# Kernel tuning notes

Measured on AMD Instinct MI355X. Metric: run time of the kernel, lower is better.

Reference implementation:

```python
import jax, jax.numpy as jnp
import numpy as np

KH, KW = 3, 3
PAD = 1
STRIDE = 1


def dht1(x):
    # 1D Discrete Hartley Transform along last axis: Re(FFT) - Im(FFT)
    f = jnp.fft.fft(x, axis=-1)
    return f.real - f.imag


def dht2(x, fft_h, fft_w):
    # zero-pad trailing two dims up to (fft_h, fft_w), then DHT along w then h
    pad_h = fft_h - x.shape[-2]
    pad_w = fft_w - x.shape[-1]
    pads = [(0, 0)] * (x.ndim - 2) + [(0, pad_h), (0, pad_w)]
    x = jnp.pad(x, pads)
    x = dht1(x)
    x = jnp.swapaxes(dht1(jnp.swapaxes(x, -1, -2)), -1, -2)
    return x


def setup_inputs() -> dict:
    key = jax.random.key(0)
    k1, k2 = jax.random.split(key)
    x = jax.random.normal(k1, (8, 64, 128, 128), dtype=jnp.float32)
    weight = jax.random.normal(k2, (64, 64, KH, KW), dtype=jnp.float32)
    return {"x": x, "weight": weight}


def reference(x, weight):
    b, c_in, h, w = x.shape
    out_h = (h + 2 * PAD - KH) // STRIDE + 1
    out_w = (w + 2 * PAD - KW) // STRIDE + 1
    x_p = jnp.pad(x, ((0, 0), (0, 0), (PAD, PAD), (PAD, PAD)))
    fft_h = h + 2 * PAD + KH - 1
    fft_w = w + 2 * PAD + KW - 1

    x_ht = dht2(x_p, fft_h, fft_w)          # [B, Cin, fh, fw]
    w_ht = dht2(weight, fft_h, fft_w)        # [Cout, Cin, fh, fw]

    x_f = jnp.flip(x_ht, axis=(-2, -1))
    w_f = jnp.flip(w_ht, axis=(-2, -1))

    # Fused combine + sum over Cin: avoids [B,Cout,Cin,fh,fw] intermediates.
    t1 = jnp.einsum('bchw,ochw->bohw', x_ht, w_ht)
    t2 = jnp.einsum('bchw,ochw->bohw', x_ht, w_f)
    t3 = jnp.einsum('bchw,ochw->bohw', x_f, w_ht)
    t4 = jnp.einsum('bchw,ochw->bohw', x_f, w_f)
    out_ht = (t1 + t2 + t3 - t4) * 0.5

    # idht2 in the source applies only the 1/n scaling twice (no transform)
    output = out_ht / jnp.asarray(fft_h * fft_w, dtype=out_ht.dtype)
    return output[:, :, :out_h, :out_w]
```

## Files before the change

### kernel.cpp

```cpp
#include <hip/hip_runtime.h>
#include <hip/hip_fp16.h>


#define SCALE (0.5f / 17424.0f)
#define MFMA  __builtin_amdgcn_mfma_f32_16x16x32_f16

typedef __attribute__((ext_vector_type(8))) _Float16 f16x8;
typedef __attribute__((ext_vector_type(4))) _Float16 f16x4;
typedef __attribute__((ext_vector_type(4))) float    f32x4;

static __device__ __forceinline__ f16x8 scl(f16x8 a, _Float16 s) {
    #pragma unroll
    for (int e = 0; e < 8; ++e) a[e] *= s;
    return a;
}

__global__ __launch_bounds__(256) void build_all(
    const float* __restrict__ w, _Float16* __restrict__ Tf,
    _Float16* __restrict__ cfT, _Float16* __restrict__ hgT)
{
    const int bid = blockIdx.x;
    const int tid = threadIdx.x;
    const float step = 6.28318530717958647692f / 132.0f;
    if (bid < 144) {
        if (tid < 128) {
            float val = 0.f;
            if (bid < 132) {
                const int m = (bid * (tid + 1)) % 132;
                float s, c;
                sincosf((float)m * step, &s, &c);
                val = c + s;
            }
            Tf[bid * 128 + tid] = (_Float16)val;
        }
        return;
    }
    if (bid == 144) {
        if (tid < 128) {
            const int v = tid;
            float s, c;
            _Float16 o[8];
            o[0] = (_Float16)1.0f; o[3] = (_Float16)1.0f;
            o[6] = (_Float16)0.0f; o[7] = (_Float16)0.0f;
            sincosf((float)((v * 1) % 132) * step, &s, &c);       o[1] = (_Float16)(c + s);
            sincosf((float)((v * 2) % 132) * step, &s, &c);       o[2] = (_Float16)(c + s);
            sincosf((float)(((v + 1) * 1) % 132) * step, &s, &c); o[4] = (_Float16)(c - s);
            sincosf((float)(((v + 1) * 2) % 132) * step, &s, &c); o[5] = (_Float16)(c - s);
            *(f16x8*)(cfT + v * 8) = *(f16x8*)o;
        }
        return;
    }
    const int bid2 = bid - 145;
    const int u = bid2 >> 2;
    const int itbase = (bid2 & 3) * 4;
    float a[3], ap[3];
    a[0] = 1.f; ap[0] = 1.f;
    #pragma unroll
    for (int i = 1; i < 3; ++i) {
        float s, c;
        sincosf((float)((u * i) % 132) * step, &s, &c);
        a[i] = c + s;
        sincosf((float)(((u + 1) * i) % 132) * step, &s, &c);
        ap[i] = c - s;
    }
    for (int it = itbase; it < itbase + 4; ++it) {
        const int oc = it * 256 + tid;
        const float* wp = w + (size_t)oc * 9;
        float w9[9];
        #pragma unroll
        for (int q = 0; q < 9; ++q) w9[q] = wp[q];
        #pragma unroll
        for (int j = 0; j < 3; ++j) {
            const float h = a[0]*w9[j] + a[1]*w9[3+j] + a[2]*w9[6+j];
            const float g = ap[0]*w9[j] + ap[1]*w9[3+j] + ap[2]*w9[6+j];
            hgT[((size_t)u * 6 + j)     * 4096 + oc] = (_Float16)h;
            hgT[((size_t)u * 6 + 3 + j) * 4096 + oc] = (_Float16)g;
        }
    }
}

__global__ __launch_bounds__(256, 2) void dht2_fused(
    const float* __restrict__ x, const _Float16* __restrict__ Tf,
    _Float16* __restrict__ X)
{
    const int bc = blockIdx.x;
    const int tid = threadIdx.x, wv = tid >> 6, lane = tid & 63;
    const int col = lane & 15, quad = lane >> 4;
    __shared__ _Float16 Tfl[144][136];
    __shared__ _Float16 Y1l[144][136];

    const float* xp = x + (size_t)bc * 16384;

    float4 xv[2][4][2];
    #pragma unroll
    for (int nt = 0; nt < 2; ++nt) {
        const int ic = (wv * 2 + nt) * 16 + col;
        #pragma unroll
        for (int kc = 0; kc < 4; ++kc) {
            const int k0 = kc * 32 + quad * 8;
            xv[nt][kc][0] = *(const float4*)(xp + ic * 128 + k0);
            xv[nt][kc][1] = *(const float4*)(xp + ic * 128 + k0 + 4);
        }
    }
    #pragma unroll
    for (int s = 0; s < 9; ++s) {
        const int idx = tid + 256 * s;
        const int row = idx >> 4;
        const int ce  = (idx & 15) * 8;
        *(f16x8*)&Tfl[row][ce] = *(const f16x8*)(Tf + (size_t)idx * 8);
    }
    f16x8 bfA[2][4];
    #pragma unroll
    for (int nt = 0; nt < 2; ++nt)
        #pragma unroll
        for (int kc = 0; kc < 4; ++kc) {
            f16x8 t;
            t[0] = (_Float16)xv[nt][kc][0].x; t[1] = (_Float16)xv[nt][kc][0].y;
            t[2] = (_Float16)xv[nt][kc][0].z; t[3] = (_Float16)xv[nt][kc][0].w;
            t[4] = (_Float16)xv[nt][kc][1].x; t[5] = (_Float16)xv[nt][kc][1].y;
            t[6] = (_Float16)xv[nt][kc][1].z; t[7] = (_Float16)xv[nt][kc][1].w;
            bfA[nt][kc] = t;
        }
    __syncthreads();

    f32x4 accA[2][9];
    #pragma unroll
    for (int nt = 0; nt < 2; ++nt)
        #pragma unroll
        for (int mt = 0; mt < 9; ++mt) accA[nt][mt] = (f32x4)0.f;
    #pragma unroll
    for (int kc = 0; kc < 4; ++kc) {
        const int k0 = kc * 32 + quad * 8;
        #pragma unroll
        for (int mt = 0; mt < 9; ++mt) {
            const f16x8 af = *(const f16x8*)&Tfl[mt * 16 + col][k0];
            accA[0][mt] = MFMA(af, bfA[0][kc], accA[0][mt], 0, 0, 0);
            accA[1][mt] = MFMA(af, bfA[1][kc], accA[1][mt], 0, 0, 0);
        }
    }
    #pragma unroll
    for (int nt = 0; nt < 2; ++nt) {
        const int ic = (wv * 2 + nt) * 16 + col;
        #pragma unroll
        for (int mt = 0; mt < 9; ++mt)
            #pragma unroll
            for (int r = 0; r < 4; ++r)
                Y1l[mt * 16 + quad * 4 + r][ic] = (_Float16)accA[nt][mt][r];
    }
    __syncthreads();

    f32x4 accB[3][9];
    #pragma unroll
    for (int t = 0; t < 3; ++t)
        #pragma unroll
        for (int mt = 0; mt < 9; ++mt) accB[t][mt] = (f32x4)0.f;
    #pragma unroll
    for (int kc = 0; kc < 4; ++kc) {
        const int k0 = kc * 32 + quad * 8;
        f16x8 af9[9];
        #pragma unroll
        for (int mt = 0; mt < 9; ++mt)
            af9[mt] = *(const f16x8*)&Tfl[mt * 16 + col][k0];
        #pragma unroll
        for (int t = 0; t < 3; ++t) {
            const int nt = wv + 4 * t;
            if (nt < 9) {
                const f16x8 bf = *(const f16x8*)&Y1l[nt * 16 + col][k0];
                #pragma unroll
                for (int mt = 0; mt < 9; ++mt)
                    accB[t][mt] = MFMA(af9[mt], bf, accB[t][mt], 0, 0, 0);
            }
        }
    }

    __syncthreads();
    #pragma unroll
    for (int t = 0; t < 3; ++t) {
        const int nt = wv + 4 * t;
        if (nt < 9) {
            const int vg = nt * 16 + col;
            if (vg < 132) {
                #pragma unroll
                for (int mt = 0; mt < 9; ++mt)
                    #pragma unroll
                    for (int r = 0; r < 4; ++r) {
                        const int u = mt * 16 + quad * 4 + r;
                        if (u < 132) Tfl[u][vg] = (_Float16)accB[t][mt][r];
                    }
            }
        }
    }
    __syncthreads();
    _Float16* Xp = X + (size_t)bc * 17952;
    #pragma unroll
    for (int k = 0; k < 9; ++k) {
        const int ch = tid + 256 * k;
        if (ch < 2244) {
            const int u = ch / 17, kk = ch - u * 17;
            *(f16x8*)(Xp + u * 136 + kk * 8) = *(const f16x8*)&Tfl[u][kk * 8];
        }
    }
}

__global__ __launch_bounds__(256) void combine_mfma(
    const _Float16* __restrict__ X, const _Float16* __restrict__ hgT,
    const _Float16* __restrict__ cfT, float* __restrict__ out)
{
    const int uidx = blockIdx.x;
    const int b = blockIdx.y;
    const int tid = threadIdx.x;
    const int wv = tid >> 6, lane = tid & 63;
    const int col = lane & 15, quad = lane >> 4;
    const int u2 = 131 - uidx;
    const bool doB = (uidx >= 4);

    __shared__ _Float16 Ps[132][72];
    __shared__ _Float16 Ms[132][72];

    {
        const int c = tid >> 2, sub = tid & 3;
        const _Float16* rowd = X + (size_t)(b * 64 + c) * 17952 + (size_t)uidx * 136;
        const _Float16* rowm = X + (size_t)(b * 64 + c) * 17952 + (size_t)u2 * 136;
        #pragma unroll
        for (int k = 0; k < 8; ++k) {
            const int v0 = sub * 32 + 4 * k;
            const f16x4 d = *(const f16x4*)(rowd + v0);
            const f16x4 m = *(const f16x4*)(rowm + (128 - v0));
            #pragma unroll
            for (int i = 0; i < 4; ++i) {
                Ps[v0 + i][c] = d[i] + m[3 - i];
                Ms[v0 + i][c] = d[i] - m[3 - i];
            }
        }
        if (sub == 0) {
            const f16x4 d = *(const f16x4*)(rowd + 128);
            const f16x4 m = *(const f16x4*)(rowm);
            #pragma unroll
            for (int i = 0; i < 4; ++i) {
                Ps[128 + i][c] = d[i] + m[3 - i];
                Ms[128 + i][c] = d[i] - m[3 - i];
            }
        }
    }
    f16x8 cfv[8];
    #pragma unroll
    for (int nt = 0; nt < 8; ++nt)
        cfv[nt] = *(const f16x8*)(cfT + (size_t)(nt * 16 + col) * 8);

    const _Float16* hgu = hgT + (size_t)uidx * 6 * 4096;
    const int orow = wv * 16 + col;
    f16x8 hA[3][2], gA[3][2];
    #pragma unroll
    for (int kt = 0; kt < 3; ++kt)
        #pragma unroll
        for (int hf = 0; hf < 2; ++hf) {
            hA[kt][hf] = *(const f16x8*)(hgu + ((size_t)kt * 64 + orow) * 64 + hf * 32 + quad * 8);
            gA[kt][hf] = *(const f16x8*)(hgu + ((size_t)(3 + kt) * 64 + orow) * 64 + hf * 32 + quad * 8);
        }
    __syncthreads();

    float* outA = out + (((size_t)(b * 64 + wv * 16 + quad * 4)) * 128 + uidx) * 128 + col;
    float* outB = out + (((size_t)(b * 64 + wv * 16 + quad * 4)) * 128 + u2) * 128 + col;

    #pragma unroll
    for (int nt = 0; nt < 8; ++nt) {
        const int vA = nt * 16 + col;
        const int vB = 131 - vA;
        const _Float16 csP1 = cfv[nt][1], csP2 = cfv[nt][2];
        const _Float16 csM1 = cfv[nt][4], csM2 = cfv[nt][5];
        {
            const f16x8 p0 = *(const f16x8*)&Ps[vA][quad * 8];
            const f16x8 p1 = *(const f16x8*)&Ps[vA][32 + quad * 8];
            const f16x8 m0 = *(const f16x8*)&Ms[vA][quad * 8];
            const f16x8 m1 = *(const f16x8*)&Ms[vA][32 + quad * 8];
            f32x4 aP = (f32x4)0.f, aM = (f32x4)0.f;
            aP = MFMA(hA[0][0], p0, aP, 0, 0, 0);
            aP = MFMA(hA[0][1], p1, aP, 0, 0, 0);
            aM = MFMA(gA[0][0], m0, aM, 0, 0, 0);
            aM = MFMA(gA[0][1], m1, aM, 0, 0, 0);
            aP = MFMA(hA[1][0], scl(p0, csP1), aP, 0, 0, 0);
            aP = MFMA(hA[1][1], scl(p1, csP1), aP, 0, 0, 0);
            aM = MFMA(gA[1][0], scl(m0, csM1), aM, 0, 0, 0);
            aM = MFMA(gA[1][1], scl(m1, csM1), aM, 0, 0, 0);
            aP = MFMA(hA[2][0], scl(p0, csP2), aP, 0, 0, 0);
            aP = MFMA(hA[2][1], scl(p1, csP2), aP, 0, 0, 0);
            aM = MFMA(gA[2][0], scl(m0, csM2), aM, 0, 0, 0);
            aM = MFMA(gA[2][1], scl(m1, csM2), aM, 0, 0, 0);
            #pragma unroll
            for (int r = 0; r < 4; ++r)
                outA[(size_t)r * 16384 + nt * 16] = (aP[r] + aM[r]) * SCALE;
        }
        if (doB) {
            const f16x8 p0 = *(const f16x8*)&Ps[vB][quad * 8];
            const f16x8 p1 = *(const f16x8*)&Ps[vB][32 + quad * 8];
            const f16x8 m0 = *(const f16x8*)&Ms[vB][quad * 8];
            const f16x8 m1 = *(const f16x8*)&Ms[vB][32 + quad * 8];
            f32x4 bP = (f32x4)0.f, bM = (f32x4)0.f;
            bP = MFMA(gA[0][0], p0, bP, 0, 0, 0);
            bP = MFMA(gA[0][1], p1, bP, 0, 0, 0);
            bM = MFMA(hA[0][0], m0, bM, 0, 0, 0);
            bM = MFMA(hA[0][1], m1, bM, 0, 0, 0);
            bP = MFMA(gA[1][0], scl(p0, csP1), bP, 0, 0, 0);
            bP = MFMA(gA[1][1], scl(p1, csP1), bP, 0, 0, 0);
            bM = MFMA(hA[1][0], scl(m0, csM1), bM, 0, 0, 0);
            bM = MFMA(hA[1][1], scl(m1, csM1), bM, 0, 0, 0);
            bP = MFMA(gA[2][0], scl(p0, csP2), bP, 0, 0, 0);
            bP = MFMA(gA[2][1], scl(p1, csP2), bP, 0, 0, 0);
            bM = MFMA(hA[2][0], scl(m0, csM2), bM, 0, 0, 0);
            bM = MFMA(hA[2][1], scl(m1, csM2), bM, 0, 0, 0);
            #pragma unroll
            for (int r = 0; r < 4; ++r)
                outB[(size_t)r * 16384 + nt * 16] = (bP[r] - bM[r]) * SCALE;
        }
    }
}

extern "C" void kernel_launch(void* const* d_in, const int* in_sizes, int n_in,
                              void* d_out, int out_size, void* d_ws, size_t ws_size,
                              hipStream_t stream)
{
    const float* x = (const float*)d_in[0];
    const float* w = (const float*)d_in[1];
    char* ws = (char*)d_ws;
    _Float16* Tf  = (_Float16*)(ws);
    _Float16* cfT = (_Float16*)(ws + 36864);
    _Float16* X   = (_Float16*)(ws + 65536);
    _Float16* hgT = (_Float16*)(ws + 18448384);

    build_all<<<dim3(409), dim3(256), 0, stream>>>(w, Tf, cfT, hgT);

    dht2_fused<<<dim3(512), dim3(256), 0, stream>>>(x, Tf, X);

    combine_mfma<<<dim3(66, 8), dim3(256), 0, stream>>>(
        X, hgT, cfT, (float*)d_out);
}
```

Before: 114.4 us.

## Widen DHT and combine kernels to 512 threads and move twiddle scaling post-MFMA

The DHT kernel now runs 8 waves per block, one 16-column tile per wave, with the leftover 132-column tail split across the first four waves. The combine kernel packs two batches into each 512-thread block with double shared buffers. It also applies the cos/sin twiddle factors in fp32 after separate MFMA accumulators, where before it scaled fp16 inputs ahead of each MFMA. The aim is less per-thread register pressure, more waves in flight and no fp16 vector scaling, at the cost of extra accumulators and roughly double the LDS per combine block.

Result: no change. 115.5 us (+1.0%).

```diff
diff --git a/kernel.cpp b/kernel.cpp
--- a/kernel.cpp
+++ b/kernel.cpp
@@ -8,12 +8,6 @@
 typedef __attribute__((ext_vector_type(8))) _Float16 f16x8;
 typedef __attribute__((ext_vector_type(4))) _Float16 f16x4;
 typedef __attribute__((ext_vector_type(4))) float    f32x4;
-
-static __device__ __forceinline__ f16x8 scl(f16x8 a, _Float16 s) {
-    #pragma unroll
-    for (int e = 0; e < 8; ++e) a[e] *= s;
-    return a;
-}
 
 __global__ __launch_bounds__(256) void build_all(
     const float* __restrict__ w, _Float16* __restrict__ Tf,
@@ -79,7 +73,7 @@
     }
 }
 
-__global__ __launch_bounds__(256, 2) void dht2_fused(
+__global__ __launch_bounds__(512, 4) void dht2_fused(
     const float* __restrict__ x, const _Float16* __restrict__ Tf,
     _Float16* __restrict__ X)
 {
@@ -90,111 +84,109 @@
     __shared__ _Float16 Y1l[144][136];
 
     const float* xp = x + (size_t)bc * 16384;
-
-    float4 xv[2][4][2];
-    #pragma unroll
-    for (int nt = 0; nt < 2; ++nt) {
-        const int ic = (wv * 2 + nt) * 16 + col;
+    const int ic = wv * 16 + col;
+
+    float4 xv[4][2];
+    #pragma unroll
+    for (int kc = 0; kc < 4; ++kc) {
+        const int k0 = kc * 32 + quad * 8;
+        xv[kc][0] = *(const float4*)(xp + ic * 128 + k0);
+        xv[kc][1] = *(const float4*)(xp + ic * 128 + k0 + 4);
+    }
+    #pragma unroll
+    for (int s = 0; s < 5; ++s) {
+        const int idx = tid + 512 * s;
+        if (idx < 2304) {
+            const int row = idx >> 4;
+            const int ce  = (idx & 15) * 8;
+            *(f16x8*)&Tfl[row][ce] = *(const f16x8*)(Tf + (size_t)idx * 8);
+        }
+    }
+    f16x8 bfA[4];
+    #pragma unroll
+    for (int kc = 0; kc < 4; ++kc) {
+        f16x8 t;
+        t[0] = (_Float16)xv[kc][0].x; t[1] = (_Float16)xv[kc][0].y;
+        t[2] = (_Float16)xv[kc][0].z; t[3] = (_Float16)xv[kc][0].w;
+        t[4] = (_Float16)xv[kc][1].x; t[5] = (_Float16)xv[kc][1].y;
+        t[6] = (_Float16)xv[kc][1].z; t[7] = (_Float16)xv[kc][1].w;
+        bfA[kc] = t;
+    }
+    __syncthreads();
+
+    f32x4 accA[9];
+    #pragma unroll
+    for (int mt = 0; mt < 9; ++mt) accA[mt] = (f32x4)0.f;
+    #pragma unroll
+    for (int kc = 0; kc < 4; ++kc) {
+        const int k0 = kc * 32 + quad * 8;
+        #pragma unroll
+        for (int mt = 0; mt < 9; ++mt) {
+            const f16x8 af = *(const f16x8*)&Tfl[mt * 16 + col][k0];
+            accA[mt] = MFMA(af, bfA[kc], accA[mt], 0, 0, 0);
+        }
+    }
+    #pragma unroll
+    for (int mt = 0; mt < 9; ++mt)
+        #pragma unroll
+        for (int r = 0; r < 4; ++r)
+            Y1l[mt * 16 + quad * 4 + r][ic] = (_Float16)accA[mt][r];
+    __syncthreads();
+
+    f32x4 accB[9];
+    #pragma unroll
+    for (int mt = 0; mt < 9; ++mt) accB[mt] = (f32x4)0.f;
+    #pragma unroll
+    for (int kc = 0; kc < 4; ++kc) {
+        const int k0 = kc * 32 + quad * 8;
+        const f16x8 bf = *(const f16x8*)&Y1l[wv * 16 + col][k0];
+        #pragma unroll
+        for (int mt = 0; mt < 9; ++mt) {
+            const f16x8 af = *(const f16x8*)&Tfl[mt * 16 + col][k0];
+            accB[mt] = MFMA(af, bf, accB[mt], 0, 0, 0);
+        }
+    }
+    f32x4 accT[3];
+    #pragma unroll
+    for (int j = 0; j < 3; ++j) accT[j] = (f32x4)0.f;
+    if (wv < 4) {
         #pragma unroll
         for (int kc = 0; kc < 4; ++kc) {
             const int k0 = kc * 32 + quad * 8;
-            xv[nt][kc][0] = *(const float4*)(xp + ic * 128 + k0);
-            xv[nt][kc][1] = *(const float4*)(xp + ic * 128 + k0 + 4);
-        }
-    }
-    #pragma unroll
-    for (int s = 0; s < 9; ++s) {
-        const int idx = tid + 256 * s;
-        const int row = idx >> 4;
-        const int ce  = (idx & 15) * 8;
-        *(f16x8*)&Tfl[row][ce] = *(const f16x8*)(Tf + (size_t)idx * 8);
-    }
-    f16x8 bfA[2][4];
-    #pragma unroll
-    for (int nt = 0; nt < 2; ++nt)
-        #pragma unroll
-        for (int kc = 0; kc < 4; ++kc) {
-            f16x8 t;
-            t[0] = (_Float16)xv[nt][kc][0].x; t[1] = (_Float16)xv[nt][kc][0].y;
-            t[2] = (_Float16)xv[nt][kc][0].z; t[3] = (_Float16)xv[nt][kc][0].w;
-            t[4] = (_Float16)xv[nt][kc][1].x; t[5] = (_Float16)xv[nt][kc][1].y;
-            t[6] = (_Float16)xv[nt][kc][1].z; t[7] = (_Float16)xv[nt][kc][1].w;
-            bfA[nt][kc] = t;
-        }
-    __syncthreads();
-
-    f32x4 accA[2][9];
-    #pragma unroll
-    for (int nt = 0; nt < 2; ++nt)
-        #pragma unroll
-        for (int mt = 0; mt < 9; ++mt) accA[nt][mt] = (f32x4)0.f;
-    #pragma unroll
-    for (int kc = 0; kc < 4; ++kc) {
-        const int k0 = kc * 32 + quad * 8;
-        #pragma unroll
-        for (int mt = 0; mt < 9; ++mt) {
-            const f16x8 af = *(const f16x8*)&Tfl[mt * 16 + col][k0];
-            accA[0][mt] = MFMA(af, bfA[0][kc], accA[0][mt], 0, 0, 0);
-            accA[1][mt] = MFMA(af, bfA[1][kc], accA[1][mt], 0, 0, 0);
-        }
-    }
-    #pragma unroll
-    for (int nt = 0; nt < 2; ++nt) {
-        const int ic = (wv * 2 + nt) * 16 + col;
-        #pragma unroll
-        for (int mt = 0; mt < 9; ++mt)
-            #pragma unroll
-            for (int r = 0; r < 4; ++r)
-                Y1l[mt * 16 + quad * 4 + r][ic] = (_Float16)accA[nt][mt][r];
-    }
-    __syncthreads();
-
-    f32x4 accB[3][9];
-    #pragma unroll
-    for (int t = 0; t < 3; ++t)
-        #pragma unroll
-        for (int mt = 0; mt < 9; ++mt) accB[t][mt] = (f32x4)0.f;
-    #pragma unroll
-    for (int kc = 0; kc < 4; ++kc) {
-        const int k0 = kc * 32 + quad * 8;
-        f16x8 af9[9];
-        #pragma unroll
-        for (int mt = 0; mt < 9; ++mt)
-            af9[mt] = *(const f16x8*)&Tfl[mt * 16 + col][k0];
-        #pragma unroll
-        for (int t = 0; t < 3; ++t) {
-            const int nt = wv + 4 * t;
-            if (nt < 9) {
-                const f16x8 bf = *(const f16x8*)&Y1l[nt * 16 + col][k0];
+            const f16x8 bf = *(const f16x8*)&Y1l[128 + col][k0];
+            #pragma unroll
+            for (int j = 0; j < 3; ++j) {
+                if (j < 2 || wv == 0) {
+                    const int mt = (j == 2) ? 8 : (wv * 2 + j);
+                    const f16x8 af = *(const f16x8*)&Tfl[mt * 16 + col][k0];
+                    accT[j] = MFMA(af, bf, accT[j], 0, 0, 0);
+                }
+            }
+        }
+    }
+    __syncthreads();
+
+    #pragma unroll
+    for (int mt = 0; mt < 9; ++mt)
+        #pragma unroll
+        for (int r = 0; r < 4; ++r)
+            Tfl[mt * 16 + quad * 4 + r][wv * 16 + col] = (_Float16)accB[mt][r];
+    if (wv < 4 && col < 4) {
+        #pragma unroll
+        for (int j = 0; j < 3; ++j) {
+            if (j < 2 || wv == 0) {
+                const int mt = (j == 2) ? 8 : (wv * 2 + j);
                 #pragma unroll
-                for (int mt = 0; mt < 9; ++mt)
-                    accB[t][mt] = MFMA(af9[mt], bf, accB[t][mt], 0, 0, 0);
-            }
-        }
-    }
-
-    __syncthreads();
-    #pragma unroll
-    for (int t = 0; t < 3; ++t) {
-        const int nt = wv + 4 * t;
-        if (nt < 9) {
-            const int vg = nt * 16 + col;
-            if (vg < 132) {
-                #pragma unroll
-                for (int mt = 0; mt < 9; ++mt)
-                    #pragma unroll
-                    for (int r = 0; r < 4; ++r) {
-                        const int u = mt * 16 + quad * 4 + r;
-                        if (u < 132) Tfl[u][vg] = (_Float16)accB[t][mt][r];
-                    }
+                for (int r = 0; r < 4; ++r)
+                    Tfl[mt * 16 + quad * 4 + r][128 + col] = (_Float16)accT[j][r];
             }
         }
     }
     __syncthreads();
     _Float16* Xp = X + (size_t)bc * 17952;
     #pragma unroll
-    for (int k = 0; k < 9; ++k) {
-        const int ch = tid + 256 * k;
+    for (int s = 0; s < 5; ++s) {
+        const int ch = tid + 512 * s;
         if (ch < 2244) {
             const int u = ch / 17, kk = ch - u * 17;
             *(f16x8*)(Xp + u * 136 + kk * 8) = *(const f16x8*)&Tfl[u][kk * 8];
@@ -202,23 +194,27 @@
     }
 }
 
-__global__ __launch_bounds__(256) void combine_mfma(
+__global__ __launch_bounds__(512, 2) void combine_mfma(
     const _Float16* __restrict__ X, const _Float16* __restrict__ hgT,
     const _Float16* __restrict__ cfT, float* __restrict__ out)
 {
     const int uidx = blockIdx.x;
-    const int b = blockIdx.y;
     const int tid = threadIdx.x;
-    const int wv = tid >> 6, lane = tid & 63;
+    const int wv8 = tid >> 6;
+    const int half = wv8 >> 2;
+    const int wv = wv8 & 3;
+    const int lane = tid & 63;
     const int col = lane & 15, quad = lane >> 4;
+    const int b = blockIdx.y * 2 + half;
     const int u2 = 131 - uidx;
     const bool doB = (uidx >= 4);
 
-    __shared__ _Float16 Ps[132][72];
-    __shared__ _Float16 Ms[132][72];
+    __shared__ _Float16 Ps[2][132][72];
+    __shared__ _Float16 Ms[2][132][72];
 
     {
-        const int c = tid >> 2, sub = tid & 3;
+        const int th = tid & 255;
+        const int c = th >> 2, sub = th & 3;
         const _Float16* rowd = X + (size_t)(b * 64 + c) * 17952 + (size_t)uidx * 136;
         const _Float16* rowm = X + (size_t)(b * 64 + c) * 17952 + (size_t)u2 * 136;
         #pragma unroll
@@ -228,8 +224,8 @@
             const f16x4 m = *(const f16x4*)(rowm + (128 - v0));
             #pragma unroll
             for (int i = 0; i < 4; ++i) {
-                Ps[v0 + i][c] = d[i] + m[3 - i];
-                Ms[v0 + i][c] = d[i] - m[3 - i];
+                Ps[half][v0 + i][c] = d[i] + m[3 - i];
+                Ms[half][v0 + i][c] = d[i] - m[3 - i];
             }
         }
         if (sub == 0) {
@@ -237,15 +233,11 @@
             const f16x4 m = *(const f16x4*)(rowm);
             #pragma unroll
             for (int i = 0; i < 4; ++i) {
-                Ps[128 + i][c] = d[i] + m[3 - i];
-                Ms[128 + i][c] = d[i] - m[3 - i];
-            }
-        }
-    }
-    f16x8 cfv[8];
-    #pragma unroll
-    for (int nt = 0; nt < 8; ++nt)
-        cfv[nt] = *(const f16x8*)(cfT + (size_t)(nt * 16 + col) * 8);
+                Ps[half][128 + i][c] = d[i] + m[3 - i];
+                Ms[half][128 + i][c] = d[i] - m[3 - i];
+            }
+        }
+    }
 
     const _Float16* hgu = hgT + (size_t)uidx * 6 * 4096;
     const int orow = wv * 16 + col;
@@ -266,51 +258,46 @@
     for (int nt = 0; nt < 8; ++nt) {
         const int vA = nt * 16 + col;
         const int vB = 131 - vA;
-        const _Float16 csP1 = cfv[nt][1], csP2 = cfv[nt][2];
-        const _Float16 csM1 = cfv[nt][4], csM2 = cfv[nt][5];
+        const f16x8 cf8 = *(const f16x8*)(cfT + (size_t)(nt * 16 + col) * 8);
+        const float c1 = (float)cf8[1], c2 = (float)cf8[2];
+        const float d1 = (float)cf8[4], d2 = (float)cf8[5];
         {
-            const f16x8 p0 = *(const f16x8*)&Ps[vA][quad * 8];
-            const f16x8 p1 = *(const f16x8*)&Ps[vA][32 + quad * 8];
-            const f16x8 m0 = *(const f16x8*)&Ms[vA][quad * 8];
-            const f16x8 m1 = *(const f16x8*)&Ms[vA][32 + quad * 8];
-            f32x4 aP = (f32x4)0.f, aM = (f32x4)0.f;
-            aP = MFMA(hA[0][0], p0, aP, 0, 0, 0);
-            aP = MFMA(hA[0][1], p1, aP, 0, 0, 0);
-            aM = MFMA(gA[0][0], m0, aM, 0, 0, 0);
-            aM = MFMA(gA[0][1], m1, aM, 0, 0, 0);
-            aP = MFMA(hA[1][0], scl(p0, csP1), aP, 0, 0, 0);
-            aP = MFMA(hA[1][1], scl(p1, csP1), aP, 0, 0, 0);
-            aM = MFMA(gA[1][0], scl(m0, csM1), aM, 0, 0, 0);
-            aM = MFMA(gA[1][1], scl(m1, csM1), aM, 0, 0, 0);
-            aP = MFMA(hA[2][0], scl(p0, csP2), aP, 0, 0, 0);
-            aP = MFMA(hA[2][1], scl(p1, csP2), aP, 0, 0, 0);
-            aM = MFMA(gA[2][0], scl(m0, csM2), aM, 0, 0, 0);
-            aM = MFMA(gA[2][1], scl(m1, csM2), aM, 0, 0, 0);
+            const f16x8 p0 = *(const f16x8*)&Ps[half][vA][quad * 8];
+            const f16x8 p1 = *(const f16x8*)&Ps[half][vA][32 + quad * 8];
+            const f16x8 m0 = *(const f16x8*)&Ms[half][vA][quad * 8];
+            const f16x8 m1 = *(const f16x8*)&Ms[half][vA][32 + quad * 8];
+            f32x4 aP0 = (f32x4)0.f, aP1 = (f32x4)0.f, aP2 = (f32x4)0.f;
+            f32x4 aM0 = (f32x4)0.f, aM1 = (f32x4)0.f, aM2 = (f32x4)0.f;
+            aP0 = MFMA(hA[0][0], p0, aP0, 0, 0, 0); aP0 = MFMA(hA[0][1], p1, aP0, 0, 0, 0);
+            aP1 = MFMA(hA[1][0], p0, aP1, 0, 0, 0); aP1 = MFMA(hA[1][1], p1, aP1, 0, 0, 0);
+            aP2 = MFMA(hA[2][0], p0, aP2, 0, 0, 0); aP2 = MFMA(hA[2][1], p1, aP2, 0, 0, 0);
+            aM0 = MFMA(gA[0][0], m0, aM0, 0, 0, 0); aM0 = MFMA(gA[0][1], m1, aM0, 0, 0, 0);
+            aM1 = MFMA(gA[1][0], m0, aM1, 0, 0, 0); aM1 = MFMA(gA[1][1], m1, aM1, 0, 0, 0);
+            aM2 = MFMA(gA[2][0], m0, aM2, 0, 0, 0); aM2 = MFMA(gA[2][1], m1, aM2, 0, 0, 0);
             #pragma unroll
             for (int r = 0; r < 4; ++r)
-                outA[(size_t)r * 16384 + nt * 16] = (aP[r] + aM[r]) * SCALE;
+                outA[(size_t)r * 16384 + nt * 16] =
+                    ((aP0[r] + c1 * aP1[r] + c2 * aP2[r]) +
+                     (aM0[r] + d1 * aM1[r] + d2 * aM2[r])) * SCALE;
         }
         if (doB) {
-            const f16x8 p0 = *(const f16x8*)&Ps[vB][quad * 8];
-            const f16x8 p1 = *(const f16x8*)&Ps[vB][32 + quad * 8];
-            const f16x8 m0 = *(const f16x8*)&Ms[vB][quad * 8];
-            const f16x8 m1 = *(const f16x8*)&Ms[vB][32 + quad * 8];
-            f32x4 bP = (f32x4)0.f, bM = (f32x4)0.f;
-            bP = MFMA(gA[0][0], p0, bP, 0, 0, 0);
-            bP = MFMA(gA[0][1], p1, bP, 0, 0, 0);
-            bM = MFMA(hA[0][0], m0, bM, 0, 0, 0);
-            bM = MFMA(hA[0][1], m1, bM, 0, 0, 0);
-            bP = MFMA(gA[1][0], scl(p0, csP1), bP, 0, 0, 0);
-            bP = MFMA(gA[1][1], scl(p1, csP1), bP, 0, 0, 0);
-            bM = MFMA(hA[1][0], scl(m0, csM1), bM, 0, 0, 0);
-            bM = MFMA(hA[1][1], scl(m1, csM1), bM, 0, 0, 0);
-            bP = MFMA(gA[2][0], scl(p0, csP2), bP, 0, 0, 0);
-            bP = MFMA(gA[2][1], scl(p1, csP2), bP, 0, 0, 0);
-            bM = MFMA(hA[2][0], scl(m0, csM2), bM, 0, 0, 0);
-            bM = MFMA(hA[2][1], scl(m1, csM2), bM, 0, 0, 0);
+            const f16x8 p0 = *(const f16x8*)&Ps[half][vB][quad * 8];
+            const f16x8 p1 = *(const f16x8*)&Ps[half][vB][32 + quad * 8];
+            const f16x8 m0 = *(const f16x8*)&Ms[half][vB][quad * 8];
+            const f16x8 m1 = *(const f16x8*)&Ms[half][vB][32 + quad * 8];
+            f32x4 bP0 = (f32x4)0.f, bP1 = (f32x4)0.f, bP2 = (f32x4)0.f;
+            f32x4 bM0 = (f32x4)0.f, bM1 = (f32x4)0.f, bM2 = (f32x4)0.f;
+            bP0 = MFMA(gA[0][0], p0, bP0, 0, 0, 0); bP0 = MFMA(gA[0][1], p1, bP0, 0, 0, 0);
+            bP1 = MFMA(gA[1][0], p0, bP1, 0, 0, 0); bP1 = MFMA(gA[1][1], p1, bP1, 0, 0, 0);
+            bP2 = MFMA(gA[2][0], p0, bP2, 0, 0, 0); bP2 = MFMA(gA[2][1], p1, bP2, 0, 0, 0);
+            bM0 = MFMA(hA[0][0], m0, bM0, 0, 0, 0); bM0 = MFMA(hA[0][1], m1, bM0, 0, 0, 0);
+            bM1 = MFMA(hA[1][0], m0, bM1, 0, 0, 0); bM1 = MFMA(hA[1][1], m1, bM1, 0, 0, 0);
+            bM2 = MFMA(hA[2][0], m0, bM2, 0, 0, 0); bM2 = MFMA(hA[2][1], m1, bM2, 0, 0, 0);
             #pragma unroll
             for (int r = 0; r < 4; ++r)
-                outB[(size_t)r * 16384 + nt * 16] = (bP[r] - bM[r]) * SCALE;
+                outB[(size_t)r * 16384 + nt * 16] =
+                    ((bP0[r] + c1 * bP1[r] + c2 * bP2[r]) -
+                     (bM0[r] + d1 * bM1[r] + d2 * bM2[r])) * SCALE;
         }
     }
 }
@@ -329,8 +316,8 @@
 
     build_all<<<dim3(409), dim3(256), 0, stream>>>(w, Tf, cfT, hgT);
 
-    dht2_fused<<<dim3(512), dim3(256), 0, stream>>>(x, Tf, X);
-
-    combine_mfma<<<dim3(66, 8), dim3(256), 0, stream>>>(
+    dht2_fused<<<dim3(512), dim3(512), 0, stream>>>(x, Tf, X);
+
+    combine_mfma<<<dim3(66, 4), dim3(512), 0, stream>>>(
         X, hgT, cfT, (float*)d_out);
 }
```
